# Optimization experiments

Measured on AMD Instinct MI355X. Metric: run time of the kernel, lower is better.

The kernel has to match this reference:

```python
import jax, jax.numpy as jnp
import numpy as np

B, Q, K, H, DQ, DK, DV = 8, 256, 256, 256, 256, 256, 256


def setup_inputs() -> dict:
    key = jax.random.key(0)
    k1, k2, k3, k4, k5, k6, k7 = jax.random.split(key, 7)
    queries = jax.random.normal(k1, (B, Q, DQ), dtype=jnp.float32)
    keys = jax.random.normal(k2, (B, K, DK), dtype=jnp.float32)
    values = jax.random.normal(k3, (B, K, DV), dtype=jnp.float32)
    valid_lens = jax.random.randint(k4, (B,), 1, K + 1)
    # learned params (torch Linear without bias); stored as (in, out)
    s = 1.0 / np.sqrt(H)
    W_q = jax.random.uniform(k5, (DQ, H), minval=-s, maxval=s, dtype=jnp.float32)
    W_k = jax.random.uniform(k6, (DK, H), minval=-s, maxval=s, dtype=jnp.float32)
    w_v = jax.random.uniform(k7, (H,), minval=-s, maxval=s, dtype=jnp.float32)
    return {"queries": queries, "keys": keys, "values": values,
            "valid_lens": valid_lens, "W_q": W_q, "W_k": W_k, "w_v": w_v}


def reference(queries, keys, values, valid_lens, W_q, W_k, w_v):
    q = queries @ W_q                      # (B, Q, H)
    k = keys @ W_k                         # (B, K, H)
    # broadcast add + tanh -> (B, Q, K, H), then linear score -> (B, Q, K)
    features = jnp.tanh(q[:, :, None, :] + k[:, None, :, :])
    scores = jnp.einsum('bqkh,h->bqk', features, w_v)
    mask = jnp.arange(K)[None, None, :] >= valid_lens[:, None, None]  # (B,1,K)
    scores = jnp.where(mask, -1000000.0, scores)
    attn = jax.nn.softmax(scores, axis=-1)  # (B, Q, K)
    return jnp.einsum('bqk,bkd->bqd', attn, values)  # (B, Q, DV)
```

## Files before the change

### kernel.cpp

```cpp
#include <hip/hip_runtime.h>
#include <hip/hip_bf16.h>

#define LOG2E 1.4426950408889634f
#define C2    (2.0f * LOG2E)

static __device__ __forceinline__ float fast_exp2(float x) {
#if __has_builtin(__builtin_amdgcn_exp2f)
  return __builtin_amdgcn_exp2f(x);
#else
  return exp2f(x);
#endif
}
static __device__ __forceinline__ float fast_rcp(float x) {
#if __has_builtin(__builtin_amdgcn_rcpf)
  return __builtin_amdgcn_rcpf(x);
#else
  return 1.0f / x;
#endif
}

typedef short bf16x8 __attribute__((ext_vector_type(8)));
typedef float f32x4  __attribute__((ext_vector_type(4)));

static __device__ __forceinline__ short f2bf(float x) {
  unsigned u = __float_as_uint(x);
  u += 0x7fff + ((u >> 16) & 1);
  return (short)(u >> 16);
}

__global__ __launch_bounds__(256, 4) void proj_kernel(
    const float* __restrict__ queries, const float* __restrict__ keys,
    const float* __restrict__ W_q,     const float* __restrict__ W_k,
    const int*   __restrict__ vlen,
    float* __restrict__ qs, float* __restrict__ ks_p)
{
  const int bz = blockIdx.z;
  const float* X = bz ? keys : queries;
  const float* W = bz ? W_k  : W_q;
  const int n0 = blockIdx.x * 16;
  const int m0 = blockIdx.y * 64;

  if (bz == 1) {
    const int vl = vlen[m0 >> 8];
    if ((m0 & 255) >= vl) return;
  }

  const int t = threadIdx.x;
  const int l = t & 63;
  const int w = t >> 6;

  __shared__ short Wp[8 * 64 * 8];

  {
    const int krow = t >> 2, nseg = t & 3;
#pragma unroll
    for (int p = 0; p < 4; ++p) {
      const int k = p * 64 + krow;
      float4 v = *(const float4*)&W[k * 256 + n0 + nseg * 4];
      const int kc = k >> 5, grp = (k & 31) >> 3, j = k & 7;
      const int lbase = grp * 16 + nseg * 4;
      Wp[(kc * 64 + lbase + 0) * 8 + j] = f2bf(v.x);
      Wp[(kc * 64 + lbase + 1) * 8 + j] = f2bf(v.y);
      Wp[(kc * 64 + lbase + 2) * 8 + j] = f2bf(v.z);
      Wp[(kc * 64 + lbase + 3) * 8 + j] = f2bf(v.w);
    }
  }
  __syncthreads();

  const int mb   = m0 + w * 16;
  const int row  = mb + (l & 15);
  const int kofs = (l >> 4) * 8;

  f32x4 acc = {0.f, 0.f, 0.f, 0.f};
#pragma unroll
  for (int kc = 0; kc < 8; ++kc) {
    float4 a0 = *(const float4*)&X[(size_t)row * 256 + kc * 32 + kofs];
    float4 a1 = *(const float4*)&X[(size_t)row * 256 + kc * 32 + kofs + 4];
    bf16x8 af;
    af[0] = f2bf(a0.x); af[1] = f2bf(a0.y); af[2] = f2bf(a0.z); af[3] = f2bf(a0.w);
    af[4] = f2bf(a1.x); af[5] = f2bf(a1.y); af[6] = f2bf(a1.z); af[7] = f2bf(a1.w);
    bf16x8 bfv = *(bf16x8*)&Wp[(kc * 64 + l) * 8];
    acc = __builtin_amdgcn_mfma_f32_16x16x32_bf16(af, bfv, acc, 0, 0, 0);
  }

  const int c = l & 15;
#pragma unroll
  for (int j = 0; j < 4; ++j) {
    const int rj = (l >> 4) * 4 + j;
    const float o = fast_exp2(acc[j] * C2);
    if (bz == 0) {
      qs[(size_t)(mb + rj) * 256 + n0 + c] = o;
    } else {
      const int b  = mb >> 8;
      const int kl = (mb & 255) + rj;
      ks_p[((size_t)(b * 64 + ((n0 + c) >> 2)) * 256 + kl) * 4 + (c & 3)] = o;
    }
  }
}

template <int NJ>
__device__ __forceinline__ void score_loop(
    const float* __restrict__ kp,
    const float* __restrict__ qp0, const float* __restrict__ qp1,
    const float* __restrict__ wvp, int h4b, float (&sc)[4][2])
{
#pragma unroll 2
  for (int h4 = h4b; h4 < h4b + 16; ++h4) {
    float4 kv[NJ];
#pragma unroll
    for (int j = 0; j < NJ; ++j)
      kv[j] = *(const float4*)(kp + h4 * 1024 + j * 256);
    float4 qv0 = *(const float4*)(qp0 + h4 * 4);
    float4 qv1 = *(const float4*)(qp1 + h4 * 4);
    float4 wv  = *(const float4*)(wvp + h4 * 4);
#pragma unroll
    for (int j = 0; j < NJ; ++j) {
      sc[j][0] = fmaf(wv.x, fast_rcp(fmaf(qv0.x, kv[j].x, 1.f)), sc[j][0]);
      sc[j][1] = fmaf(wv.x, fast_rcp(fmaf(qv1.x, kv[j].x, 1.f)), sc[j][1]);
      sc[j][0] = fmaf(wv.y, fast_rcp(fmaf(qv0.y, kv[j].y, 1.f)), sc[j][0]);
      sc[j][1] = fmaf(wv.y, fast_rcp(fmaf(qv1.y, kv[j].y, 1.f)), sc[j][1]);
      sc[j][0] = fmaf(wv.z, fast_rcp(fmaf(qv0.z, kv[j].z, 1.f)), sc[j][0]);
      sc[j][1] = fmaf(wv.z, fast_rcp(fmaf(qv1.z, kv[j].z, 1.f)), sc[j][1]);
      sc[j][0] = fmaf(wv.w, fast_rcp(fmaf(qv0.w, kv[j].w, 1.f)), sc[j][0]);
      sc[j][1] = fmaf(wv.w, fast_rcp(fmaf(qv1.w, kv[j].w, 1.f)), sc[j][1]);
    }
  }
}

__global__ __launch_bounds__(256, 4) void attn_kernel(
    const float* __restrict__ qs, const float* __restrict__ ks_p,
    const float* __restrict__ values, const int* __restrict__ vlen,
    const float* __restrict__ w_v, float* __restrict__ out)
{
  const int t    = threadIdx.x;
  const int lane = t & 63;
  const int hq   = t >> 6;
  const int bx   = blockIdx.x;
  const int b    = ((bx & 7) + (bx >> 8)) & 7;
  const int q0   = (bx >> 3) * 2;

  __shared__ __align__(16) float sbuf[2048];
  __shared__ __align__(8)  float p2[512];
  __shared__ float rsum_lds[2];

  const int vl = vlen[b];
  const int nj = (vl + 63) >> 6;

  float s0 = w_v[lane] + w_v[lane + 64] + w_v[lane + 128] + w_v[lane + 192];
#pragma unroll
  for (int off = 32; off; off >>= 1) s0 += __shfl_xor(s0, off);
  const float Wsum = s0;

  const float* qp0 = qs + (size_t)(b * 256 + q0) * 256;
  const float* qp1 = qp0 + 256;
  const float* kp  = ks_p + (size_t)b * 65536 + lane * 4;
  const int h4b = hq * 16;

  float sc[4][2] = {};
  switch (nj) {
    case 1:  score_loop<1>(kp, qp0, qp1, w_v, h4b, sc); break;
    case 2:  score_loop<2>(kp, qp0, qp1, w_v, h4b, sc); break;
    case 3:  score_loop<3>(kp, qp0, qp1, w_v, h4b, sc); break;
    default: score_loop<4>(kp, qp0, qp1, w_v, h4b, sc); break;
  }

#pragma unroll
  for (int j = 0; j < 4; ++j)
    *(float2*)&sbuf[((hq * 4 + j) * 64 + lane) * 2] =
        make_float2(sc[j][0], sc[j][1]);
  __syncthreads();

  if (hq < 2) {
    const int q = hq;
    float scores[4];
    float mx = -3.4e38f;
#pragma unroll 4
    for (int j = 0; j < nj; ++j) {
      float s = sbuf[((0 * 4 + j) * 64 + lane) * 2 + q] +
                sbuf[((1 * 4 + j) * 64 + lane) * 2 + q] +
                sbuf[((2 * 4 + j) * 64 + lane) * 2 + q] +
                sbuf[((3 * 4 + j) * 64 + lane) * 2 + q];
      float v = Wsum - 2.f * s;
      if (j * 64 + lane >= vl) v = -1000000.0f;
      scores[j] = v;
      mx = fmaxf(mx, v);
    }
#pragma unroll
    for (int off = 32; off; off >>= 1) mx = fmaxf(mx, __shfl_xor(mx, off));
    float sum = 0.f;
#pragma unroll 4
    for (int j = 0; j < nj; ++j) {
      float p = fast_exp2((scores[j] - mx) * LOG2E);
      p2[(j * 64 + lane) * 2 + q] = p;
      sum += p;
    }
#pragma unroll
    for (int off = 32; off; off >>= 1) sum += __shfl_xor(sum, off);
    if (lane == 0) rsum_lds[q] = sum;
  }
  __syncthreads();

  float4 a0 = make_float4(0.f, 0.f, 0.f, 0.f);
  float4 a1 = make_float4(0.f, 0.f, 0.f, 0.f);
  const float* Vb = values + (size_t)b * 65536 + lane * 4;
#pragma unroll 2
  for (int k = hq; k < vl; k += 4) {
    float2 pk = *(const float2*)&p2[k * 2];
    float4 v  = *(const float4*)(Vb + (size_t)k * 256);
    a0.x = fmaf(pk.x, v.x, a0.x);
    a0.y = fmaf(pk.x, v.y, a0.y);
    a0.z = fmaf(pk.x, v.z, a0.z);
    a0.w = fmaf(pk.x, v.w, a0.w);
    a1.x = fmaf(pk.y, v.x, a1.x);
    a1.y = fmaf(pk.y, v.y, a1.y);
    a1.z = fmaf(pk.y, v.z, a1.z);
    a1.w = fmaf(pk.y, v.w, a1.w);
  }
  *(float4*)&sbuf[(hq * 2 + 0) * 256 + lane * 4] = a0;
  *(float4*)&sbuf[(hq * 2 + 1) * 256 + lane * 4] = a1;
  __syncthreads();

#pragma unroll
  for (int rep = 0; rep < 2; ++rep) {
    int o = t + rep * 256;
    int q = o >> 8, d = o & 255;
    float s = sbuf[(0 + q) * 256 + d] + sbuf[(2 + q) * 256 + d] +
              sbuf[(4 + q) * 256 + d] + sbuf[(6 + q) * 256 + d];
    out[(b * 256 + q0 + q) * 256 + d] = s * fast_rcp(rsum_lds[q]);
  }
}

extern "C" void kernel_launch(void* const* d_in, const int* in_sizes, int n_in,
                              void* d_out, int out_size, void* d_ws, size_t ws_size,
                              hipStream_t stream) {
  const float* queries = (const float*)d_in[0];
  const float* keys    = (const float*)d_in[1];
  const float* values  = (const float*)d_in[2];
  const int*   vlenp   = (const int*)d_in[3];
  const float* W_q     = (const float*)d_in[4];
  const float* W_k     = (const float*)d_in[5];
  const float* w_v     = (const float*)d_in[6];
  float* out = (float*)d_out;

  float* qs   = (float*)d_ws;
  float* ks_p = qs + 2048 * 256;

  dim3 pgrid(16, 32, 2);
  proj_kernel<<<pgrid, 256, 0, stream>>>(queries, keys, W_q, W_k, vlenp, qs, ks_p);
  attn_kernel<<<1024, 256, 0, stream>>>(qs, ks_p, values, vlenp, w_v, out);
}
```

Baseline: 40.83 us.

## Process four queries per block with 512 threads to reuse key loads

The attention kernel now handles four query rows per block instead of two, using 8 waves that each cover 8 h4 slices. Each key element loaded feeds four queries, which halves key-projection global traffic per score. The grid shrinks to 512 blocks, and the PV loop gains software prefetch of the next value row. In exchange, register use per thread and LDS use per block go up (sbuf grows to 32KB), which may reduce occupancy, and fewer blocks may leave some CUs with less work.

```diff
diff --git a/kernel.cpp b/kernel.cpp
--- a/kernel.cpp
+++ b/kernel.cpp
@@ -98,50 +98,51 @@
   }
 }
 
+#define SC_STEP(c)                                                         \
+  sc[j][0] = fmaf(wv.c, fast_rcp(fmaf(qv0.c, kv[j].c, 1.f)), sc[j][0]);    \
+  sc[j][1] = fmaf(wv.c, fast_rcp(fmaf(qv1.c, kv[j].c, 1.f)), sc[j][1]);    \
+  sc[j][2] = fmaf(wv.c, fast_rcp(fmaf(qv2.c, kv[j].c, 1.f)), sc[j][2]);    \
+  sc[j][3] = fmaf(wv.c, fast_rcp(fmaf(qv3.c, kv[j].c, 1.f)), sc[j][3]);
+
 template <int NJ>
 __device__ __forceinline__ void score_loop(
     const float* __restrict__ kp,
-    const float* __restrict__ qp0, const float* __restrict__ qp1,
-    const float* __restrict__ wvp, int h4b, float (&sc)[4][2])
+    const float* __restrict__ qp,
+    const float* __restrict__ wvp, int h4b, float (&sc)[4][4])
 {
 #pragma unroll 2
-  for (int h4 = h4b; h4 < h4b + 16; ++h4) {
+  for (int h4 = h4b; h4 < h4b + 8; ++h4) {
     float4 kv[NJ];
 #pragma unroll
     for (int j = 0; j < NJ; ++j)
       kv[j] = *(const float4*)(kp + h4 * 1024 + j * 256);
-    float4 qv0 = *(const float4*)(qp0 + h4 * 4);
-    float4 qv1 = *(const float4*)(qp1 + h4 * 4);
+    float4 qv0 = *(const float4*)(qp + 0 * 256 + h4 * 4);
+    float4 qv1 = *(const float4*)(qp + 1 * 256 + h4 * 4);
+    float4 qv2 = *(const float4*)(qp + 2 * 256 + h4 * 4);
+    float4 qv3 = *(const float4*)(qp + 3 * 256 + h4 * 4);
     float4 wv  = *(const float4*)(wvp + h4 * 4);
 #pragma unroll
     for (int j = 0; j < NJ; ++j) {
-      sc[j][0] = fmaf(wv.x, fast_rcp(fmaf(qv0.x, kv[j].x, 1.f)), sc[j][0]);
-      sc[j][1] = fmaf(wv.x, fast_rcp(fmaf(qv1.x, kv[j].x, 1.f)), sc[j][1]);
-      sc[j][0] = fmaf(wv.y, fast_rcp(fmaf(qv0.y, kv[j].y, 1.f)), sc[j][0]);
-      sc[j][1] = fmaf(wv.y, fast_rcp(fmaf(qv1.y, kv[j].y, 1.f)), sc[j][1]);
-      sc[j][0] = fmaf(wv.z, fast_rcp(fmaf(qv0.z, kv[j].z, 1.f)), sc[j][0]);
-      sc[j][1] = fmaf(wv.z, fast_rcp(fmaf(qv1.z, kv[j].z, 1.f)), sc[j][1]);
-      sc[j][0] = fmaf(wv.w, fast_rcp(fmaf(qv0.w, kv[j].w, 1.f)), sc[j][0]);
-      sc[j][1] = fmaf(wv.w, fast_rcp(fmaf(qv1.w, kv[j].w, 1.f)), sc[j][1]);
-    }
-  }
-}
-
-__global__ __launch_bounds__(256, 4) void attn_kernel(
+      SC_STEP(x); SC_STEP(y); SC_STEP(z); SC_STEP(w);
+    }
+  }
+}
+
+__global__ __launch_bounds__(512, 4) void attn_kernel(
     const float* __restrict__ qs, const float* __restrict__ ks_p,
     const float* __restrict__ values, const int* __restrict__ vlen,
     const float* __restrict__ w_v, float* __restrict__ out)
 {
   const int t    = threadIdx.x;
   const int lane = t & 63;
-  const int hq   = t >> 6;
+  const int w    = t >> 6;
   const int bx   = blockIdx.x;
-  const int b    = ((bx & 7) + (bx >> 8)) & 7;
-  const int q0   = (bx >> 3) * 2;
-
-  __shared__ __align__(16) float sbuf[2048];
-  __shared__ __align__(8)  float p2[512];
-  __shared__ float rsum_lds[2];
+  const int b    = ((bx & 7) + (bx >> 6)) & 7;
+  const int q0   = (bx >> 3) * 4;
+
+  __shared__ __align__(16) float sbuf[8192];
+  __shared__ __align__(16) float p2[256 * 4];
+  __shared__ float rsum_lds[4];
 
   const int vl = vlen[b];
   const int nj = (vl + 63) >> 6;
@@ -151,35 +152,34 @@
   for (int off = 32; off; off >>= 1) s0 += __shfl_xor(s0, off);
   const float Wsum = s0;
 
-  const float* qp0 = qs + (size_t)(b * 256 + q0) * 256;
-  const float* qp1 = qp0 + 256;
-  const float* kp  = ks_p + (size_t)b * 65536 + lane * 4;
-  const int h4b = hq * 16;
-
-  float sc[4][2] = {};
+  const float* qp = qs + (size_t)(b * 256 + q0) * 256;
+  const float* kp = ks_p + (size_t)b * 65536 + lane * 4;
+  const int h4b = w * 8;
+
+  float sc[4][4] = {};
   switch (nj) {
-    case 1:  score_loop<1>(kp, qp0, qp1, w_v, h4b, sc); break;
-    case 2:  score_loop<2>(kp, qp0, qp1, w_v, h4b, sc); break;
-    case 3:  score_loop<3>(kp, qp0, qp1, w_v, h4b, sc); break;
-    default: score_loop<4>(kp, qp0, qp1, w_v, h4b, sc); break;
+    case 1:  score_loop<1>(kp, qp, w_v, h4b, sc); break;
+    case 2:  score_loop<2>(kp, qp, w_v, h4b, sc); break;
+    case 3:  score_loop<3>(kp, qp, w_v, h4b, sc); break;
+    default: score_loop<4>(kp, qp, w_v, h4b, sc); break;
   }
 
 #pragma unroll
   for (int j = 0; j < 4; ++j)
-    *(float2*)&sbuf[((hq * 4 + j) * 64 + lane) * 2] =
-        make_float2(sc[j][0], sc[j][1]);
-  __syncthreads();
-
-  if (hq < 2) {
-    const int q = hq;
+    *(float4*)&sbuf[((w * 4 + j) * 64 + lane) * 4] =
+        make_float4(sc[j][0], sc[j][1], sc[j][2], sc[j][3]);
+  __syncthreads();
+
+  if (w < 4) {
+    const int q = w;
     float scores[4];
     float mx = -3.4e38f;
 #pragma unroll 4
     for (int j = 0; j < nj; ++j) {
-      float s = sbuf[((0 * 4 + j) * 64 + lane) * 2 + q] +
-                sbuf[((1 * 4 + j) * 64 + lane) * 2 + q] +
-                sbuf[((2 * 4 + j) * 64 + lane) * 2 + q] +
-                sbuf[((3 * 4 + j) * 64 + lane) * 2 + q];
+      float s = 0.f;
+#pragma unroll
+      for (int ww = 0; ww < 8; ++ww)
+        s += sbuf[((ww * 4 + j) * 64 + lane) * 4 + q];
       float v = Wsum - 2.f * s;
       if (j * 64 + lane >= vl) v = -1000000.0f;
       scores[j] = v;
@@ -191,7 +191,7 @@
 #pragma unroll 4
     for (int j = 0; j < nj; ++j) {
       float p = fast_exp2((scores[j] - mx) * LOG2E);
-      p2[(j * 64 + lane) * 2 + q] = p;
+      p2[(j * 64 + lane) * 4 + q] = p;
       sum += p;
     }
 #pragma unroll
@@ -200,33 +200,48 @@
   }
   __syncthreads();
 
-  float4 a0 = make_float4(0.f, 0.f, 0.f, 0.f);
-  float4 a1 = make_float4(0.f, 0.f, 0.f, 0.f);
+  float4 acc[4];
+#pragma unroll
+  for (int q = 0; q < 4; ++q) acc[q] = make_float4(0.f, 0.f, 0.f, 0.f);
   const float* Vb = values + (size_t)b * 65536 + lane * 4;
-#pragma unroll 2
-  for (int k = hq; k < vl; k += 4) {
-    float2 pk = *(const float2*)&p2[k * 2];
-    float4 v  = *(const float4*)(Vb + (size_t)k * 256);
-    a0.x = fmaf(pk.x, v.x, a0.x);
-    a0.y = fmaf(pk.x, v.y, a0.y);
-    a0.z = fmaf(pk.x, v.z, a0.z);
-    a0.w = fmaf(pk.x, v.w, a0.w);
-    a1.x = fmaf(pk.y, v.x, a1.x);
-    a1.y = fmaf(pk.y, v.y, a1.y);
-    a1.z = fmaf(pk.y, v.z, a1.z);
-    a1.w = fmaf(pk.y, v.w, a1.w);
-  }
-  *(float4*)&sbuf[(hq * 2 + 0) * 256 + lane * 4] = a0;
-  *(float4*)&sbuf[(hq * 2 + 1) * 256 + lane * 4] = a1;
+  if (w < vl) {
+    float4 v = *(const float4*)(Vb + (size_t)w * 256);
+    for (int k = w; k < vl; k += 8) {
+      float4 vn = v;
+      if (k + 8 < vl) vn = *(const float4*)(Vb + (size_t)(k + 8) * 256);
+      float4 pk = *(const float4*)&p2[k * 4];
+      acc[0].x = fmaf(pk.x, v.x, acc[0].x);
+      acc[0].y = fmaf(pk.x, v.y, acc[0].y);
+      acc[0].z = fmaf(pk.x, v.z, acc[0].z);
+      acc[0].w = fmaf(pk.x, v.w, acc[0].w);
+      acc[1].x = fmaf(pk.y, v.x, acc[1].x);
+      acc[1].y = fmaf(pk.y, v.y, acc[1].y);
+      acc[1].z = fmaf(pk.y, v.z, acc[1].z);
+      acc[1].w = fmaf(pk.y, v.w, acc[1].w);
+      acc[2].x = fmaf(pk.z, v.x, acc[2].x);
+      acc[2].y = fmaf(pk.z, v.y, acc[2].y);
+      acc[2].z = fmaf(pk.z, v.z, acc[2].z);
+      acc[2].w = fmaf(pk.z, v.w, acc[2].w);
+      acc[3].x = fmaf(pk.w, v.x, acc[3].x);
+      acc[3].y = fmaf(pk.w, v.y, acc[3].y);
+      acc[3].z = fmaf(pk.w, v.z, acc[3].z);
+      acc[3].w = fmaf(pk.w, v.w, acc[3].w);
+      v = vn;
+    }
+  }
+#pragma unroll
+  for (int q = 0; q < 4; ++q)
+    *(float4*)&sbuf[(w * 4 + q) * 256 + lane * 4] = acc[q];
   __syncthreads();
 
 #pragma unroll
   for (int rep = 0; rep < 2; ++rep) {
-    int o = t + rep * 256;
+    int o = t + rep * 512;
     int q = o >> 8, d = o & 255;
-    float s = sbuf[(0 + q) * 256 + d] + sbuf[(2 + q) * 256 + d] +
-              sbuf[(4 + q) * 256 + d] + sbuf[(6 + q) * 256 + d];
-    out[(b * 256 + q0 + q) * 256 + d] = s * fast_rcp(rsum_lds[q]);
+    float s = 0.f;
+#pragma unroll
+    for (int ww = 0; ww < 8; ++ww) s += sbuf[(ww * 4 + q) * 256 + d];
+    out[(size_t)(b * 256 + q0 + q) * 256 + d] = s * fast_rcp(rsum_lds[q]);
   }
 }
 
@@ -247,5 +262,5 @@
 
   dim3 pgrid(16, 32, 2);
   proj_kernel<<<pgrid, 256, 0, stream>>>(queries, keys, W_q, W_k, vlenp, qs, ks_p);
-  attn_kernel<<<1024, 256, 0, stream>>>(qs, ks_p, values, vlenp, w_v, out);
-}
+  attn_kernel<<<512, 512, 0, stream>>>(qs, ks_p, values, vlenp, w_v, out);
+}
```

Result: faster. 38.98 us (-4.5%).
